# Kernel tuning notes

Measured on AMD Instinct MI355X. Metric: run time of the kernel, lower is better.

## Reference

```python
import jax, jax.numpy as jnp
import numpy as np

N_NODES = 50000
N_EDGES = 800000
NEG_SLOPE = 0.2  # leaky_relu slope used in the model


def setup_inputs() -> dict:
    key = jax.random.key(0)
    ks = jax.random.split(key, 8)
    d_in, d_h, d_out = 64, 64, 4
    x = jax.random.normal(ks[0], (N_NODES, d_in), dtype=jnp.float32)
    edge_index = jax.random.randint(ks[1], (2, N_EDGES), 0, N_NODES, dtype=jnp.int32)
    # Glorot-style init like PyG GCNConv
    W0 = jax.random.normal(ks[2], (d_in, d_h), dtype=jnp.float32) * np.float32(1.0 / np.sqrt(d_in))
    W1 = jax.random.normal(ks[3], (d_h, d_h), dtype=jnp.float32) * np.float32(1.0 / np.sqrt(d_h))
    W2 = jax.random.normal(ks[4], (d_h, d_out), dtype=jnp.float32) * np.float32(1.0 / np.sqrt(d_h))
    b0 = jnp.zeros((d_h,), dtype=jnp.float32)
    b1 = jnp.zeros((d_h,), dtype=jnp.float32)
    b2 = jnp.zeros((d_out,), dtype=jnp.float32)
    return {"x": x, "edge_index": edge_index, "W0": W0, "b0": b0,
            "W1": W1, "b1": b1, "W2": W2, "b2": b2}


def _gcn_norm(edge_index, n_nodes, dtype):
    # Add self-loops, compute symmetric normalization D^{-1/2} (A+I) D^{-1/2}
    src, dst = edge_index[0], edge_index[1]
    loop = jnp.arange(n_nodes, dtype=src.dtype)
    src = jnp.concatenate([src, loop])
    dst = jnp.concatenate([dst, loop])
    deg = jax.ops.segment_sum(jnp.ones_like(dst, dtype=dtype), dst, num_segments=n_nodes)
    dinv = jnp.where(deg > 0, jax.lax.rsqrt(deg), jnp.zeros_like(deg))
    norm = dinv[src] * dinv[dst]  # [E + N]
    return src, dst, norm


def _gcn_layer(h, src, dst, norm, W, b, n_nodes):
    h = h @ W                                  # [N, d_out]
    msg = h[src] * norm[:, None]               # gather + edge scaling
    out = jax.ops.segment_sum(msg, dst, num_segments=n_nodes)  # scatter-add
    return out + b


def reference(x, edge_index, W0, b0, W1, b1, W2, b2):
    # Eval-mode forward: dropout_edge and F.dropout are identity when not training.
    n = x.shape[0]
    src, dst, norm = _gcn_norm(edge_index, n, x.dtype)
    h = _gcn_layer(x, src, dst, norm, W0, b0, n)
    h = jax.nn.leaky_relu(h, NEG_SLOPE)
    h = _gcn_layer(h, src, dst, norm, W1, b1, n)
    h = jax.nn.leaky_relu(h, NEG_SLOPE)
    out = _gcn_layer(h, src, dst, norm, W2, b2, n)
    return out
```

## Files before the change

kernel.cpp:

```cpp
#include <hip/hip_runtime.h>
#include <math.h>

#define NEG_SLOPE 0.2f
#define NPAD 50176
#define NW8  (NPAD / 4)
#define NCHUNK 256

__global__ __launch_bounds__(1024) void k_hist(const int* __restrict__ dst,
                                               unsigned int* __restrict__ histw,
                                               unsigned char* __restrict__ rank,
                                               int e, int es) {
    extern __shared__ unsigned int lcnt[];
    int t = threadIdx.x;
    for (int w = t; w < NW8; w += 1024) lcnt[w] = 0u;
    __syncthreads();
    int beg = blockIdx.x * es;
    int end = min(beg + es, e);
    for (int i = beg + t; i < end; i += 1024) {
        int d = dst[i];
        int sh = (d & 3) << 3;
        unsigned int old = atomicAdd(&lcnt[d >> 2], 1u << sh);
        rank[i] = (unsigned char)((old >> sh) & 0xffu);
    }
    __syncthreads();
    unsigned int* out = histw + (size_t)blockIdx.x * NW8;
    for (int w = t; w < NW8; w += 1024) out[w] = lcnt[w];
}

__global__ __launch_bounds__(256) void k_chscan(unsigned char* __restrict__ hist8,
                                                float* __restrict__ dinv,
                                                unsigned short* __restrict__ deg16,
                                                int* __restrict__ bsum, int n) {
    int t = threadIdx.x;
    int i = blockIdx.x * 256 + t;
    unsigned char* p = hist8 + i;
    unsigned int run = 0;
    for (int c = 0; c < NCHUNK; c += 8) {
        size_t b = (size_t)c * NPAD;
        unsigned char v0 = p[b];
        unsigned char v1 = p[b + (size_t)1 * NPAD];
        unsigned char v2 = p[b + (size_t)2 * NPAD];
        unsigned char v3 = p[b + (size_t)3 * NPAD];
        unsigned char v4 = p[b + (size_t)4 * NPAD];
        unsigned char v5 = p[b + (size_t)5 * NPAD];
        unsigned char v6 = p[b + (size_t)6 * NPAD];
        unsigned char v7 = p[b + (size_t)7 * NPAD];
        unsigned int e0 = run;
        unsigned int e1 = e0 + v0;
        unsigned int e2 = e1 + v1;
        unsigned int e3 = e2 + v2;
        unsigned int e4 = e3 + v3;
        unsigned int e5 = e4 + v4;
        unsigned int e6 = e5 + v5;
        unsigned int e7 = e6 + v6;
        run = e7 + v7;
        p[b] = (unsigned char)e0;
        p[b + (size_t)1 * NPAD] = (unsigned char)e1;
        p[b + (size_t)2 * NPAD] = (unsigned char)e2;
        p[b + (size_t)3 * NPAD] = (unsigned char)e3;
        p[b + (size_t)4 * NPAD] = (unsigned char)e4;
        p[b + (size_t)5 * NPAD] = (unsigned char)e5;
        p[b + (size_t)6 * NPAD] = (unsigned char)e6;
        p[b + (size_t)7 * NPAD] = (unsigned char)e7;
    }
    int deg = (int)run;
    if (i < n) dinv[i] = rsqrtf((float)(deg + 1));
    deg16[i] = (unsigned short)deg;
    int s = deg;
    for (int d = 1; d < 64; d <<= 1) s += __shfl_down(s, d);
    __shared__ int ws[4];
    if ((t & 63) == 0) ws[t >> 6] = s;
    __syncthreads();
    if (t == 0) bsum[blockIdx.x] = ws[0] + ws[1] + ws[2] + ws[3];
}

__global__ __launch_bounds__(256) void k_scan3(const unsigned short* __restrict__ deg16,
                                               const int* __restrict__ bsum,
                                               int* __restrict__ rowptr, int n, int nb) {
    __shared__ int ls[256];
    __shared__ int wo[4];
    int t = threadIdx.x;
    int bid = blockIdx.x;
    int bv = (t < bid && t < nb) ? bsum[t] : 0;
    for (int d = 1; d < 64; d <<= 1) bv += __shfl_down(bv, d);
    if ((t & 63) == 0) wo[t >> 6] = bv;
    __syncthreads();
    int boff = wo[0] + wo[1] + wo[2] + wo[3];
    int i = bid * 256 + t;
    int v = (i < n) ? (int)deg16[i] : 0;
    ls[t] = v;
    __syncthreads();
    for (int d = 1; d < 256; d <<= 1) {
        int u = (t >= d) ? ls[t - d] : 0;
        __syncthreads();
        ls[t] += u;
        __syncthreads();
    }
    int excl = ls[t] - v + boff;
    if (i < n) rowptr[i] = excl;
    if (i == n - 1) rowptr[n] = excl + v;
}

__global__ void k_place(const int* __restrict__ src, const int* __restrict__ dst,
                        const int* __restrict__ rowptr, const unsigned char* __restrict__ rank,
                        const unsigned char* __restrict__ choff,
                        int* __restrict__ perm, int e, int es) {
    int i = blockIdx.x * 256 + threadIdx.x;
    if (i >= e) return;
    int d = dst[i];
    unsigned int c = (unsigned int)i / (unsigned int)es;
    int slot = rowptr[d] + (int)choff[(size_t)c * NPAD + d] + (int)rank[i];
    perm[slot] = src[i];
}

__global__ __launch_bounds__(256) void k_gemm64(const float* __restrict__ in,
                                                const float* __restrict__ W,
                                                const float* __restrict__ dinv,
                                                _Float16* __restrict__ out, int n) {
    __shared__ float Ws[64 * 64];
    __shared__ float Xs[16 * 64];
    int t = threadIdx.x;
    const float4* W4 = (const float4*)W;
    float4* Ws4 = (float4*)Ws;
#pragma unroll
    for (int i = 0; i < 4; ++i) Ws4[t + 256 * i] = W4[t + 256 * i];
    int row0 = blockIdx.x * 16;
    {
        int r = t >> 4, c4 = t & 15;
        int row = row0 + r;
        float4 v = make_float4(0.f, 0.f, 0.f, 0.f);
        if (row < n) v = ((const float4*)(in + (size_t)row * 64))[c4];
        ((float4*)Xs)[t] = v;
    }
    __syncthreads();
    int c = t & 63, g = t >> 6;
    float a0 = 0.f, a1 = 0.f, a2 = 0.f, a3 = 0.f;
#pragma unroll
    for (int k = 0; k < 64; ++k) {
        float w = Ws[k * 64 + c];
        a0 = fmaf(Xs[g * 64 + k], w, a0);
        a1 = fmaf(Xs[(g + 4) * 64 + k], w, a1);
        a2 = fmaf(Xs[(g + 8) * 64 + k], w, a2);
        a3 = fmaf(Xs[(g + 12) * 64 + k], w, a3);
    }
    int r;
    r = row0 + g;      if (r < n) out[(size_t)r * 64 + c] = (_Float16)(a0 * dinv[r]);
    r = row0 + g + 4;  if (r < n) out[(size_t)r * 64 + c] = (_Float16)(a1 * dinv[r]);
    r = row0 + g + 8;  if (r < n) out[(size_t)r * 64 + c] = (_Float16)(a2 * dinv[r]);
    r = row0 + g + 12; if (r < n) out[(size_t)r * 64 + c] = (_Float16)(a3 * dinv[r]);
}

__global__ __launch_bounds__(256) void k_gather64(
        const _Float16* __restrict__ h, const float* __restrict__ dinv,
        const int* __restrict__ rowptr, const int* __restrict__ perm,
        const float* __restrict__ b, float* __restrict__ out, int n, int act,
        const float* __restrict__ W2, float* __restrict__ y, int fuse) {
    int t = threadIdx.x;
    int v = blockIdx.x * 4 + (t >> 6);
    if (v >= n) return;
    v = __builtin_amdgcn_readfirstlane(v);
    int lane = t & 63;
    const _Float16* hl = h + lane;
    float acc = (float)hl[(size_t)v * 64];
    int e = rowptr[v], end = rowptr[v + 1];
#define LOADK(j) float x##j = (float)hl[(size_t)perm[e + j] * 64]
    for (; e + 16 <= end; e += 16) {
        LOADK(0); LOADK(1); LOADK(2); LOADK(3);
        LOADK(4); LOADK(5); LOADK(6); LOADK(7);
        LOADK(8); LOADK(9); LOADK(10); LOADK(11);
        LOADK(12); LOADK(13); LOADK(14); LOADK(15);
        acc += (((x0 + x1) + (x2 + x3)) + ((x4 + x5) + (x6 + x7)))
             + (((x8 + x9) + (x10 + x11)) + ((x12 + x13) + (x14 + x15)));
    }
    if (e + 8 <= end) {
        LOADK(0); LOADK(1); LOADK(2); LOADK(3);
        LOADK(4); LOADK(5); LOADK(6); LOADK(7);
        acc += ((x0 + x1) + (x2 + x3)) + ((x4 + x5) + (x6 + x7));
        e += 8;
    }
    if (e + 4 <= end) {
        LOADK(0); LOADK(1); LOADK(2); LOADK(3);
        acc += (x0 + x1) + (x2 + x3);
        e += 4;
    }
    if (e + 2 <= end) {
        LOADK(0); LOADK(1);
        acc += x0 + x1;
        e += 2;
    }
    if (e < end) acc += (float)hl[(size_t)perm[e] * 64];
#undef LOADK
    float dv = dinv[v];
    acc = acc * dv + b[lane];
    if (act) acc = acc > 0.0f ? acc : acc * NEG_SLOPE;
    if (!fuse) {
        out[(size_t)v * 64 + lane] = acc;
    } else {
        float4 w = ((const float4*)W2)[lane];
        float p0 = acc * w.x, p1 = acc * w.y, p2 = acc * w.z, p3 = acc * w.w;
#pragma unroll
        for (int dlt = 1; dlt < 64; dlt <<= 1) {
            p0 += __shfl_xor(p0, dlt);
            p1 += __shfl_xor(p1, dlt);
            p2 += __shfl_xor(p2, dlt);
            p3 += __shfl_xor(p3, dlt);
        }
        if (lane == 0)
            ((float4*)y)[v] = make_float4(p0 * dv, p1 * dv, p2 * dv, p3 * dv);
    }
}

__global__ __launch_bounds__(256) void k_gather4(
        const float* __restrict__ h, const float* __restrict__ dinv,
        const int* __restrict__ rowptr, const int* __restrict__ perm,
        const float* __restrict__ b, float* __restrict__ out, int n) {
    int gid = blockIdx.x * 256 + threadIdx.x;
    int c = gid & 3;
    int v = gid >> 2;
    if (v >= n) return;
    const float* hc = h + c;
    float acc = hc[(size_t)v * 4];
    int e = rowptr[v], end = rowptr[v + 1];
    for (; e + 4 <= end; e += 4) {
        float x0 = hc[(size_t)perm[e] * 4];
        float x1 = hc[(size_t)perm[e + 1] * 4];
        float x2 = hc[(size_t)perm[e + 2] * 4];
        float x3 = hc[(size_t)perm[e + 3] * 4];
        acc += (x0 + x1) + (x2 + x3);
    }
    for (; e < end; ++e) acc += hc[(size_t)perm[e] * 4];
    out[(size_t)v * 4 + c] = acc * dinv[v] + b[c];
}

extern "C" void kernel_launch(void* const* d_in, const int* in_sizes, int n_in,
                              void* d_out, int out_size, void* d_ws, size_t ws_size,
                              hipStream_t stream) {
    const float* x  = (const float*)d_in[0];
    const int* ei   = (const int*)d_in[1];
    const float* W0 = (const float*)d_in[2];
    const float* b0 = (const float*)d_in[3];
    const float* W1 = (const float*)d_in[4];
    const float* b1 = (const float*)d_in[5];
    const float* W2 = (const float*)d_in[6];
    const float* b2 = (const float*)d_in[7];
    float* out = (float*)d_out;

    const int N = in_sizes[0] / 64;
    const int E = in_sizes[1] / 2;
    const int* src = ei;
    const int* dst = ei + E;
    const int es = (E + NCHUNK - 1) / NCHUNK;

    char* base = (char*)d_ws;
    size_t off = 0;
    auto alloc = [&](size_t bytes) { size_t o = off; off = (off + bytes + 255) & ~(size_t)255; return o; };
    unsigned int*   histw  = (unsigned int*)(base + alloc((size_t)NCHUNK * NPAD));
    unsigned char*  rank   = (unsigned char*)(base + alloc((size_t)E));
    unsigned short* deg16  = (unsigned short*)(base + alloc((size_t)NPAD * 2));
    float*          dinv   = (float*)(base + alloc((size_t)NPAD * 4));
    int*            rowptr = (int*)(base + alloc((size_t)(NPAD + 1) * 4));
    int*            bsum   = (int*)(base + alloc(1024));
    int*            perm   = (int*)(base + alloc((size_t)E * 4));
    _Float16*       bufH   = (_Float16*)(base + alloc((size_t)N * 64 * 2));
    float*          bufB   = (float*)(base + alloc((size_t)N * 64 * 4));
    float*          bufD   = (float*)(base + alloc((size_t)N * 4 * 4));

    const int nb_N = (N + 255) / 256;
    const int nb_E = (E + 255) / 256;
    const int nb_V = (N + 3) / 4;

    k_hist<<<NCHUNK, 1024, NW8 * sizeof(unsigned int), stream>>>(dst, histw, rank, E, es);
    k_chscan<<<NPAD / 256, 256, 0, stream>>>((unsigned char*)histw, dinv, deg16, bsum, N);
    k_scan3<<<nb_N, 256, 0, stream>>>(deg16, bsum, rowptr, N, nb_N);
    k_place<<<nb_E, 256, 0, stream>>>(src, dst, rowptr, rank, (const unsigned char*)histw, perm, E, es);

    k_gemm64<<<(N + 15) / 16, 256, 0, stream>>>(x, W0, dinv, bufH, N);
    k_gather64<<<nb_V, 256, 0, stream>>>(bufH, dinv, rowptr, perm, b0, bufB, N, 1,
                                         W2, bufD, 0);

    k_gemm64<<<(N + 15) / 16, 256, 0, stream>>>(bufB, W1, dinv, bufH, N);
    k_gather64<<<nb_V, 256, 0, stream>>>(bufH, dinv, rowptr, perm, b1, bufB, N, 1,
                                         W2, bufD, 1);

    k_gather4<<<(N * 4 + 255) / 256, 256, 0, stream>>>(bufD, dinv, rowptr, perm, b2, out, N);
}
```

Before: 163.3 us.

## Recompute ranks in chunked LDS placement and store layer-1 activations as fp16

The per-edge rank byte array is gone. Edge placement now reloads each chunk's exclusive-offset histogram into shared memory and takes slots from LDS atomics, replacing the scattered per-edge reads of the byte histogram in global memory. The intermediate activations between the first gather and the second GEMM are stored in fp16 instead of fp32, which halves that buffer's traffic. The costs are a second round of LDS atomics per edge, a non-deterministic order of neighbours within each row, and some loss of precision in the intermediate.

```diff
diff --git a/kernel.cpp b/kernel.cpp
--- a/kernel.cpp
+++ b/kernel.cpp
@@ -6,9 +6,10 @@
 #define NW8  (NPAD / 4)
 #define NCHUNK 256
 
+typedef _Float16 half4 __attribute__((ext_vector_type(4)));
+
 __global__ __launch_bounds__(1024) void k_hist(const int* __restrict__ dst,
                                                unsigned int* __restrict__ histw,
-                                               unsigned char* __restrict__ rank,
                                                int e, int es) {
     extern __shared__ unsigned int lcnt[];
     int t = threadIdx.x;
@@ -18,9 +19,7 @@
     int end = min(beg + es, e);
     for (int i = beg + t; i < end; i += 1024) {
         int d = dst[i];
-        int sh = (d & 3) << 3;
-        unsigned int old = atomicAdd(&lcnt[d >> 2], 1u << sh);
-        rank[i] = (unsigned char)((old >> sh) & 0xffu);
+        atomicAdd(&lcnt[d >> 2], 1u << ((d & 3) << 3));
     }
     __syncthreads();
     unsigned int* out = histw + (size_t)blockIdx.x * NW8;
@@ -101,19 +100,29 @@
     if (i == n - 1) rowptr[n] = excl + v;
 }
 
-__global__ void k_place(const int* __restrict__ src, const int* __restrict__ dst,
-                        const int* __restrict__ rowptr, const unsigned char* __restrict__ rank,
-                        const unsigned char* __restrict__ choff,
-                        int* __restrict__ perm, int e, int es) {
-    int i = blockIdx.x * 256 + threadIdx.x;
-    if (i >= e) return;
-    int d = dst[i];
-    unsigned int c = (unsigned int)i / (unsigned int)es;
-    int slot = rowptr[d] + (int)choff[(size_t)c * NPAD + d] + (int)rank[i];
-    perm[slot] = src[i];
-}
-
-__global__ __launch_bounds__(256) void k_gemm64(const float* __restrict__ in,
+__global__ __launch_bounds__(1024) void k_place2(const int* __restrict__ src,
+                                                 const int* __restrict__ dst,
+                                                 const int* __restrict__ rowptr,
+                                                 const unsigned int* __restrict__ choffw,
+                                                 int* __restrict__ perm, int e, int es) {
+    extern __shared__ unsigned int cur[];
+    int t = threadIdx.x;
+    const unsigned int* in = choffw + (size_t)blockIdx.x * NW8;
+    for (int w = t; w < NW8; w += 1024) cur[w] = in[w];
+    __syncthreads();
+    int beg = blockIdx.x * es;
+    int end = min(beg + es, e);
+    for (int i = beg + t; i < end; i += 1024) {
+        int d = dst[i];
+        int sh = (d & 3) << 3;
+        unsigned int old = atomicAdd(&cur[d >> 2], 1u << sh);
+        int slot = rowptr[d] + (int)((old >> sh) & 0xffu);
+        perm[slot] = src[i];
+    }
+}
+
+template <typename T>
+__global__ __launch_bounds__(256) void k_gemm64(const T* __restrict__ in,
                                                 const float* __restrict__ W,
                                                 const float* __restrict__ dinv,
                                                 _Float16* __restrict__ out, int n) {
@@ -129,7 +138,14 @@
         int r = t >> 4, c4 = t & 15;
         int row = row0 + r;
         float4 v = make_float4(0.f, 0.f, 0.f, 0.f);
-        if (row < n) v = ((const float4*)(in + (size_t)row * 64))[c4];
+        if (row < n) {
+            if constexpr (sizeof(T) == 4) {
+                v = ((const float4*)(in + (size_t)row * 64))[c4];
+            } else {
+                half4 hv = ((const half4*)(in + (size_t)row * 64))[c4];
+                v = make_float4((float)hv.x, (float)hv.y, (float)hv.z, (float)hv.w);
+            }
+        }
         ((float4*)Xs)[t] = v;
     }
     __syncthreads();
@@ -153,7 +169,7 @@
 __global__ __launch_bounds__(256) void k_gather64(
         const _Float16* __restrict__ h, const float* __restrict__ dinv,
         const int* __restrict__ rowptr, const int* __restrict__ perm,
-        const float* __restrict__ b, float* __restrict__ out, int n, int act,
+        const float* __restrict__ b, _Float16* __restrict__ out, int n, int act,
         const float* __restrict__ W2, float* __restrict__ y, int fuse) {
     int t = threadIdx.x;
     int v = blockIdx.x * 4 + (t >> 6);
@@ -194,7 +210,7 @@
     acc = acc * dv + b[lane];
     if (act) acc = acc > 0.0f ? acc : acc * NEG_SLOPE;
     if (!fuse) {
-        out[(size_t)v * 64 + lane] = acc;
+        out[(size_t)v * 64 + lane] = (_Float16)acc;
     } else {
         float4 w = ((const float4*)W2)[lane];
         float p0 = acc * w.x, p1 = acc * w.y, p2 = acc * w.z, p3 = acc * w.w;
@@ -255,31 +271,29 @@
     size_t off = 0;
     auto alloc = [&](size_t bytes) { size_t o = off; off = (off + bytes + 255) & ~(size_t)255; return o; };
     unsigned int*   histw  = (unsigned int*)(base + alloc((size_t)NCHUNK * NPAD));
-    unsigned char*  rank   = (unsigned char*)(base + alloc((size_t)E));
     unsigned short* deg16  = (unsigned short*)(base + alloc((size_t)NPAD * 2));
     float*          dinv   = (float*)(base + alloc((size_t)NPAD * 4));
     int*            rowptr = (int*)(base + alloc((size_t)(NPAD + 1) * 4));
     int*            bsum   = (int*)(base + alloc(1024));
     int*            perm   = (int*)(base + alloc((size_t)E * 4));
     _Float16*       bufH   = (_Float16*)(base + alloc((size_t)N * 64 * 2));
-    float*          bufB   = (float*)(base + alloc((size_t)N * 64 * 4));
+    _Float16*       bufB16 = (_Float16*)(base + alloc((size_t)N * 64 * 2));
     float*          bufD   = (float*)(base + alloc((size_t)N * 4 * 4));
 
     const int nb_N = (N + 255) / 256;
-    const int nb_E = (E + 255) / 256;
     const int nb_V = (N + 3) / 4;
 
-    k_hist<<<NCHUNK, 1024, NW8 * sizeof(unsigned int), stream>>>(dst, histw, rank, E, es);
+    k_hist<<<NCHUNK, 1024, NW8 * sizeof(unsigned int), stream>>>(dst, histw, E, es);
     k_chscan<<<NPAD / 256, 256, 0, stream>>>((unsigned char*)histw, dinv, deg16, bsum, N);
     k_scan3<<<nb_N, 256, 0, stream>>>(deg16, bsum, rowptr, N, nb_N);
-    k_place<<<nb_E, 256, 0, stream>>>(src, dst, rowptr, rank, (const unsigned char*)histw, perm, E, es);
-
-    k_gemm64<<<(N + 15) / 16, 256, 0, stream>>>(x, W0, dinv, bufH, N);
-    k_gather64<<<nb_V, 256, 0, stream>>>(bufH, dinv, rowptr, perm, b0, bufB, N, 1,
+    k_place2<<<NCHUNK, 1024, NW8 * sizeof(unsigned int), stream>>>(src, dst, rowptr, histw, perm, E, es);
+
+    k_gemm64<float><<<(N + 15) / 16, 256, 0, stream>>>(x, W0, dinv, bufH, N);
+    k_gather64<<<nb_V, 256, 0, stream>>>(bufH, dinv, rowptr, perm, b0, bufB16, N, 1,
                                          W2, bufD, 0);
 
-    k_gemm64<<<(N + 15) / 16, 256, 0, stream>>>(bufB, W1, dinv, bufH, N);
-    k_gather64<<<nb_V, 256, 0, stream>>>(bufH, dinv, rowptr, perm, b1, bufB, N, 1,
+    k_gemm64<_Float16><<<(N + 15) / 16, 256, 0, stream>>>(bufB16, W1, dinv, bufH, N);
+    k_gather64<<<nb_V, 256, 0, stream>>>(bufH, dinv, rowptr, perm, b1, bufB16, N, 1,
                                          W2, bufD, 1);
 
     k_gather4<<<(N * 4 + 255) / 256, 256, 0, stream>>>(bufD, dinv, rowptr, perm, b2, out, N);
```

New measurement: 159.5 us. 2.3% less time.
